# Kernel tuning notes

Measured on AMD Instinct MI355X. Metric: run time of the kernel, lower is better.

## Reference

```python
import jax, jax.numpy as jnp
import numpy as np

WS = 8       # window size
NH = 6       # num heads
SHIFT = 4    # ws//2 since index=1 (shifted)
EPS = 1e-6


def _rel_pos_index(ws):
    coords = np.stack(np.meshgrid(np.arange(ws), np.arange(ws), indexing='ij'))  # (2,ws,ws)
    cf = coords.reshape(2, -1)
    rel = (cf[:, :, None] - cf[:, None, :]).transpose(1, 2, 0)  # (N,N,2)
    rel[..., 0] += ws - 1
    rel[..., 1] += ws - 1
    rel[..., 0] *= 2 * ws - 1
    return rel.sum(-1)  # (N,N) int


def _attn_mask(H, W, ws, shift):
    img = np.zeros((H, W))
    slices = (slice(0, -ws), slice(-ws, -shift), slice(-shift, None))
    cnt = 0
    for h in slices:
        for w in slices:
            img[h, w] = cnt
            cnt += 1
    mw = img.reshape(H // ws, ws, W // ws, ws).transpose(0, 2, 1, 3).reshape(-1, ws * ws)
    am = mw[:, None, :] - mw[:, :, None]  # (nW,N,N): unsqueeze(1) - unsqueeze(2)
    return np.where(am != 0, -100.0, 0.0).astype(np.float32)


def layernorm2d(x, w, b):
    mu = x.mean(1, keepdims=True)
    var = ((x - mu) ** 2).mean(1, keepdims=True)
    y = (x - mu) / jnp.sqrt(var + EPS)
    return w[None, :, None, None] * y + b[None, :, None, None]


def window_partition(x, ws):
    B, C, H, W = x.shape
    x = x.reshape(B, C, H // ws, ws, W // ws, ws)
    return x.transpose(0, 2, 4, 3, 5, 1).reshape(-1, ws * ws, C)


def window_reverse(win, ws, H, W):
    B = win.shape[0] // ((H // ws) * (W // ws))
    x = win.reshape(B, H // ws, W // ws, ws, ws, -1)
    return x.transpose(0, 5, 1, 3, 2, 4).reshape(B, -1, H, W)


def shifted_window_attn(x, qkv_w, qkv_b, proj_w, proj_b, rpb_table):
    B, C, H, W = x.shape
    N = WS * WS
    hd = C // NH
    scale = hd ** -0.5
    # faithful to original: raw reshape BCHW->BHWC (reinterpretation), roll, reshape back
    x = jnp.roll(x.reshape(B, H, W, C), (-SHIFT, -SHIFT), (1, 2)).reshape(B, C, H, W)
    win = window_partition(x, WS)  # (B_, N, C)
    B_ = win.shape[0]
    qkv = (win @ qkv_w + qkv_b).reshape(B_, N, 3, NH, hd).transpose(2, 0, 3, 1, 4)
    q, k, v = qkv[0] * scale, qkv[1], qkv[2]
    attn = jnp.einsum('bhnd,bhmd->bhnm', q, k)  # (B_,NH,N,N)
    rpi = _rel_pos_index(WS)
    bias = rpb_table[rpi.reshape(-1)].reshape(N, N, NH).transpose(2, 0, 1)
    attn = attn + bias[None]
    mask = jnp.asarray(_attn_mask(H, W, WS, SHIFT))  # (nW,N,N)
    nW = mask.shape[0]
    attn = attn.reshape(B_ // nW, nW, NH, N, N) + mask[None, :, None]
    attn = jax.nn.softmax(attn.reshape(B_, NH, N, N), axis=-1)
    out = jnp.einsum('bhnm,bhmd->bhnd', attn, v).transpose(0, 2, 1, 3).reshape(B_, N, C)
    out = out @ proj_w + proj_b
    return window_reverse(out, WS, H, W)


def channel_attention(y, ca_w, ca_b):
    gap = y.mean((2, 3))  # (B,C)
    s = jnp.einsum('bc,oc->bo', gap, ca_w) + ca_b  # 1x1 conv on pooled feature
    return s[:, :, None, None]


def mlp(y, fc1_w, fc1_b, fc2_w, fc2_b):
    B, C, H, W = y.shape
    t = y.transpose(0, 2, 3, 1)  # (B,H,W,C)
    t = jax.nn.gelu(t @ fc1_w + fc1_b, approximate=False)
    t = t @ fc2_w + fc2_b
    return t.transpose(0, 3, 1, 2)


def setup_inputs() -> dict:
    key = jax.random.key(0)
    ks = jax.random.split(key, 8)
    C, H, W, B = 192, 256, 256, 2
    hid = 2 * C
    sc = 0.02
    return {
        'x': jax.random.normal(ks[0], (B, C, H, W), jnp.float32),
        'norm1_w': jnp.ones((C,), jnp.float32),
        'norm1_b': jnp.zeros((C,), jnp.float32),
        'qkv_w': jax.random.normal(ks[1], (C, 3 * C), jnp.float32) * sc,
        'qkv_b': jnp.zeros((3 * C,), jnp.float32),
        'proj_w': jax.random.normal(ks[2], (C, C), jnp.float32) * sc,
        'proj_b': jnp.zeros((C,), jnp.float32),
        'rpb_table': jax.random.normal(ks[3], ((2 * WS - 1) ** 2, NH), jnp.float32) * sc,
        'ca_w': jax.random.normal(ks[4], (C, C), jnp.float32) * sc,
        'ca_b': jnp.zeros((C,), jnp.float32),
        'norm2_w': jnp.ones((C,), jnp.float32),
        'norm2_b': jnp.zeros((C,), jnp.float32),
        'fc1_w': jax.random.normal(ks[5], (C, hid), jnp.float32) * sc,
        'fc1_b': jnp.zeros((hid,), jnp.float32),
        'fc2_w': jax.random.normal(ks[6], (hid, C), jnp.float32) * sc,
        'fc2_b': jnp.zeros((C,), jnp.float32),
    }


def reference(x, norm1_w, norm1_b, qkv_w, qkv_b, proj_w, proj_b, rpb_table,
              ca_w, ca_b, norm2_w, norm2_b, fc1_w, fc1_b, fc2_w, fc2_b):
    y = layernorm2d(x, norm1_w, norm1_b)
    y = shifted_window_attn(y, qkv_w, qkv_b, proj_w, proj_b, rpb_table)
    y = y * channel_attention(y, ca_w, ca_b)
    x = x + y
    y2 = mlp(layernorm2d(x, norm2_w, norm2_b), fc1_w, fc1_b, fc2_w, fc2_b)
    return x + y2
```

## Files before the change

### kernel.cpp

```cpp
#include <hip/hip_runtime.h>
#include <hip/hip_bf16.h>
#include <stdint.h>

#define C_   192
#define H_   256
#define W_   256
#define HW_  65536
#define CHW  12582912
#define NH_  6
#define HID_ 384

typedef __attribute__((ext_vector_type(8))) __bf16 bf16x8;
typedef __attribute__((ext_vector_type(4))) float  fx4;

__device__ __forceinline__ uint16_t f2bf(float f) {
  uint32_t u = __builtin_bit_cast(uint32_t, f);
  u += 0x7fffu + ((u >> 16) & 1u);
  return (uint16_t)(u >> 16);
}
__device__ __forceinline__ float bf2f(uint16_t h) {
  uint32_t u = ((uint32_t)h) << 16;
  return __builtin_bit_cast(float, u);
}
__device__ __forceinline__ uint32_t pk2(float a, float b) {
  return (uint32_t)f2bf(a) | ((uint32_t)f2bf(b) << 16);
}
__device__ __forceinline__ bf16x8 ld8(const uint16_t* p) {
  uint4 v = *reinterpret_cast<const uint4*>(p);
  return __builtin_bit_cast(bf16x8, v);
}
__device__ __forceinline__ fx4 mfma16(bf16x8 a, bf16x8 b, fx4 c) {
  return __builtin_amdgcn_mfma_f32_16x16x32_bf16(a, b, c, 0, 0, 0);
}

__global__ __launch_bounds__(256) void prep_kernel(
    const float* __restrict__ qkv_w, const float* __restrict__ proj_w,
    const float* __restrict__ fc1_w, const float* __restrict__ fc2_w,
    const float* __restrict__ rpb,
    uint16_t* __restrict__ qkv_wt, uint16_t* __restrict__ proj_wt,
    uint16_t* __restrict__ fc1_wt, uint16_t* __restrict__ fc2_wt,
    float* __restrict__ rpbb) {
  int tid = blockIdx.x * 256 + threadIdx.x;
  if (tid < 576 * 192) {
    int f = tid / 192, k = tid % 192;
    qkv_wt[tid] = f2bf(qkv_w[k * 576 + f]);
  }
  int t1 = tid - 576 * 192;
  if (t1 >= 0 && t1 < 192 * 192) {
    int f = t1 / 192, k = t1 % 192;
    proj_wt[t1] = f2bf(proj_w[k * 192 + f]);
  }
  int t2 = t1 - 192 * 192;
  if (t2 >= 0 && t2 < 384 * 192) {
    int f = t2 / 192, k = t2 % 192;
    fc1_wt[t2] = f2bf(fc1_w[k * 384 + f]);
  }
  int t3 = t2 - 384 * 192;
  if (t3 >= 0 && t3 < 192 * 384) {
    int f = t3 / 384, k = t3 % 384;
    fc2_wt[t3] = f2bf(fc2_w[k * 192 + f]);
  }
  int t4 = t3 - 192 * 384;
  if (t4 >= 0 && t4 < 6 * 64 * 64) {
    int h = t4 / 4096, nm = t4 % 4096, n = nm / 64, m = nm % 64;
    int yn = n >> 3, xn = n & 7, ym = m >> 3, xm = m & 7;
    int idx = (yn - ym + 7) * 15 + (xn - xm + 7);
    rpbb[t4] = rpb[idx * NH_ + h];
  }
}

__global__ __launch_bounds__(256) void ln1_stats(const float* __restrict__ x,
                                                 float* __restrict__ mu,
                                                 float* __restrict__ rsig) {
  int t = blockIdx.x * 256 + threadIdx.x;
  int b = t >> 16, hw = t & 65535;
  const float* xp = x + (size_t)b * CHW + hw;
  float s = 0.f, sq = 0.f;
#pragma unroll 8
  for (int c = 0; c < C_; c++) {
    float v = xp[(size_t)c * HW_];
    s += v; sq += v * v;
  }
  float m = s * (1.0f / C_);
  float var = sq * (1.0f / C_) - m * m;
  mu[t] = m;
  rsig[t] = rsqrtf(var + 1e-6f);
}

__global__ __launch_bounds__(256) void ln1_apply_kernel(
    const float* __restrict__ x, const float* __restrict__ mu, const float* __restrict__ rsig,
    const float* __restrict__ n1w, const float* __restrict__ n1b,
    uint16_t* __restrict__ y_tok) {
  __shared__ __attribute__((aligned(16))) uint16_t tile[192 * 66];
  int wg = blockIdx.x;
  int b = wg >> 10, hw0 = (wg & 1023) << 6;
  int t = threadIdx.x;
  const float* xb = x + (size_t)b * CHW;
  const float* mub = mu + b * HW_;
  const float* rsb = rsig + b * HW_;
#pragma unroll 4
  for (int it = 0; it < 48; it++) {
    int id = it * 256 + t;
    int ca = id >> 6, pp = id & 63;
    int g = ca * 65536 + hw0 + pp;
    int h2 = g / 49152;
    int r = g - h2 * 49152;
    int w2 = r / 192;
    int c2 = r - w2 * 192;
    int f = ((h2 + 4) & 255) * 49152 + ((w2 + 4) & 255) * 192 + c2;
    int cnat = f >> 16;
    int hwn = f & 65535;
    float v = (xb[f] - mub[hwn]) * rsb[hwn] * n1w[cnat] + n1b[cnat];
    tile[ca * 66 + pp] = f2bf(v);
  }
  __syncthreads();
  uint16_t* yb = y_tok + ((size_t)(b * HW_ + hw0)) * C_;
#pragma unroll 4
  for (int it = 0; it < 48; it++) {
    int id = it * 256 + t;
    int pp = id / 192, ca = id - pp * 192;
    yb[id] = tile[ca * 66 + pp];
  }
}

__global__ __launch_bounds__(256, 2) void attn_kernel(
    const uint16_t* __restrict__ y_tok, const uint16_t* __restrict__ qkv_wt,
    const float* __restrict__ qkv_b, const uint16_t* __restrict__ proj_wt,
    const float* __restrict__ proj_b, const float* __restrict__ rpbb,
    uint16_t* __restrict__ y_attn) {
  __shared__ __attribute__((aligned(16))) uint16_t Qs[64 * 200];
  __shared__ __attribute__((aligned(16))) uint16_t Ks[64 * 200];
  __shared__ __attribute__((aligned(16))) uint16_t VT[32 * 72];
  __shared__ __attribute__((aligned(16))) uint16_t Ps[64 * 72];
  const int wg = blockIdx.x;
  const int b = wg >> 10, wid = wg & 1023;
  const int wh = wid >> 5, ww = wid & 31;
  const int t = threadIdx.x;
  const int w = t >> 6, l = t & 63;
  const int lane16 = l & 15, quad = l >> 4;
  const int trow = w * 16 + quad * 4;

  bf16x8 afr[4][6];
#pragma unroll
  for (int m = 0; m < 4; m++) {
    const int tok = m * 16 + lane16;
    const uint16_t* ap = y_tok +
        ((size_t)(b * HW_ + (wh * 8 + (tok >> 3)) * W_ + ww * 8 + (tok & 7))) * C_ + quad * 8;
#pragma unroll
    for (int k = 0; k < 6; k++) afr[m][k] = ld8(ap + k * 32);
  }

  const float scale = 0.17677669529663687f;
  uint32_t vpack[3][4][2];

#pragma unroll
  for (int j = 0; j < 3; j++) {
    const int nt = w + 4 * j;
    const uint16_t* bp = qkv_wt + (nt * 16 + lane16) * C_ + quad * 8;
    bf16x8 bfr[6];
#pragma unroll
    for (int k = 0; k < 6; k++) bfr[k] = ld8(bp + k * 32);
    fx4 acc[4];
#pragma unroll
    for (int m = 0; m < 4; m++) acc[m] = fx4{0.f, 0.f, 0.f, 0.f};
#pragma unroll
    for (int k = 0; k < 6; k++)
#pragma unroll
      for (int m = 0; m < 4; m++) acc[m] = mfma16(afr[m][k], bfr[k], acc[m]);
    const int f = nt * 16 + lane16;
    const float bias = qkv_b[f];
#pragma unroll
    for (int m = 0; m < 4; m++)
#pragma unroll
      for (int r = 0; r < 4; r++)
        Qs[(m * 16 + quad * 4 + r) * 200 + f] = f2bf((acc[m][r] + bias) * scale);
  }
#pragma unroll
  for (int j = 3; j < 6; j++) {
    const int nt = w + 4 * j;
    const uint16_t* bp = qkv_wt + (nt * 16 + lane16) * C_ + quad * 8;
    bf16x8 bfr[6];
#pragma unroll
    for (int k = 0; k < 6; k++) bfr[k] = ld8(bp + k * 32);
    fx4 acc[4];
#pragma unroll
    for (int m = 0; m < 4; m++) acc[m] = fx4{0.f, 0.f, 0.f, 0.f};
#pragma unroll
    for (int k = 0; k < 6; k++)
#pragma unroll
      for (int m = 0; m < 4; m++) acc[m] = mfma16(afr[m][k], bfr[k], acc[m]);
    const int f = nt * 16 + lane16;
    const float bias = qkv_b[f];
#pragma unroll
    for (int m = 0; m < 4; m++)
#pragma unroll
      for (int r = 0; r < 4; r++)
        Ks[(m * 16 + quad * 4 + r) * 200 + (f - 192)] = f2bf(acc[m][r] + bias);
  }
#pragma unroll
  for (int j = 6; j < 9; j++) {
    const int nt = w + 4 * j;
    const uint16_t* bp = qkv_wt + (nt * 16 + lane16) * C_ + quad * 8;
    bf16x8 bfr[6];
#pragma unroll
    for (int k = 0; k < 6; k++) bfr[k] = ld8(bp + k * 32);
    fx4 acc[4];
#pragma unroll
    for (int m = 0; m < 4; m++) acc[m] = fx4{0.f, 0.f, 0.f, 0.f};
#pragma unroll
    for (int k = 0; k < 6; k++)
#pragma unroll
      for (int m = 0; m < 4; m++) acc[m] = mfma16(afr[m][k], bfr[k], acc[m]);
    const float bias = qkv_b[nt * 16 + lane16];
    const int jv = j - 6;
#pragma unroll
    for (int m = 0; m < 4; m++) {
      vpack[jv][m][0] = pk2(acc[m][0] + bias, acc[m][1] + bias);
      vpack[jv][m][1] = pk2(acc[m][2] + bias, acc[m][3] + bias);
    }
  }

  const bool whe = (wh == 31), wwe = (ww == 31);

  for (int h = 0; h < 6; h++) {
    __syncthreads();
    {
      const int vt0 = 2 * h, vt1 = 2 * h + 1;
      if (w == (vt0 & 3)) {
        const int jv = vt0 >> 2;
#pragma unroll
        for (int m = 0; m < 4; m++) {
          uint2 vv; vv.x = vpack[jv][m][0]; vv.y = vpack[jv][m][1];
          *reinterpret_cast<uint2*>(&VT[lane16 * 72 + m * 16 + quad * 4]) = vv;
        }
      }
      if (w == (vt1 & 3)) {
        const int jv = vt1 >> 2;
#pragma unroll
        for (int m = 0; m < 4; m++) {
          uint2 vv; vv.x = vpack[jv][m][0]; vv.y = vpack[jv][m][1];
          *reinterpret_cast<uint2*>(&VT[(16 + lane16) * 72 + m * 16 + quad * 4]) = vv;
        }
      }
    }
    __syncthreads();

    const bf16x8 qa = ld8(&Qs[(w * 16 + lane16) * 200 + h * 32 + quad * 8]);
    fx4 sacc[4];
#pragma unroll
    for (int nt = 0; nt < 4; nt++) {
      const bf16x8 kb = ld8(&Ks[(nt * 16 + lane16) * 200 + h * 32 + quad * 8]);
      fx4 z = {0.f, 0.f, 0.f, 0.f};
      sacc[nt] = mfma16(qa, kb, z);
    }
    const float* rb = rpbb + h * 4096;
#pragma unroll
    for (int nt = 0; nt < 4; nt++) {
      const int ct = nt * 16 + lane16;
      const bool rbc = whe && ((ct >> 3) >= 4);
      const bool cbc = wwe && ((ct & 7) >= 4);
#pragma unroll
      for (int r = 0; r < 4; r++) {
        const int rt = trow + r;
        const bool rbr = whe && ((rt >> 3) >= 4);
        const bool cbr = wwe && ((rt & 7) >= 4);
        float v = sacc[nt][r] + rb[rt * 64 + ct];
        if (rbr != rbc || cbr != cbc) v -= 100.f;
        sacc[nt][r] = v;
      }
    }
    float sm[4];
#pragma unroll
    for (int r = 0; r < 4; r++) {
      float m = fmaxf(fmaxf(sacc[0][r], sacc[1][r]), fmaxf(sacc[2][r], sacc[3][r]));
      m = fmaxf(m, __shfl_xor(m, 1));
      m = fmaxf(m, __shfl_xor(m, 2));
      m = fmaxf(m, __shfl_xor(m, 4));
      m = fmaxf(m, __shfl_xor(m, 8));
      float s0 = 0.f;
#pragma unroll
      for (int nt = 0; nt < 4; nt++) {
        float e = exp2f((sacc[nt][r] - m) * 1.4426950408889634f);
        sacc[nt][r] = e; s0 += e;
      }
      s0 += __shfl_xor(s0, 1);
      s0 += __shfl_xor(s0, 2);
      s0 += __shfl_xor(s0, 4);
      s0 += __shfl_xor(s0, 8);
      sm[r] = s0;
    }
#pragma unroll
    for (int nt = 0; nt < 4; nt++)
#pragma unroll
      for (int r = 0; r < 4; r++)
        Ps[(trow + r) * 72 + nt * 16 + lane16] = f2bf(sacc[nt][r]);
    fx4 o0 = {0.f, 0.f, 0.f, 0.f}, o1 = {0.f, 0.f, 0.f, 0.f};
#pragma unroll
    for (int ks2 = 0; ks2 < 2; ks2++) {
      const bf16x8 pa = ld8(&Ps[(w * 16 + lane16) * 72 + ks2 * 32 + quad * 8]);
      const bf16x8 v0 = ld8(&VT[(lane16) * 72 + ks2 * 32 + quad * 8]);
      const bf16x8 v1 = ld8(&VT[(16 + lane16) * 72 + ks2 * 32 + quad * 8]);
      o0 = mfma16(pa, v0, o0);
      o1 = mfma16(pa, v1, o1);
    }
#pragma unroll
    for (int r = 0; r < 4; r++) {
      const float inv = 1.0f / sm[r];
      Qs[(trow + r) * 200 + h * 32 + lane16] = f2bf(o0[r] * inv);
      Qs[(trow + r) * 200 + h * 32 + 16 + lane16] = f2bf(o1[r] * inv);
    }
  }
  __syncthreads();

  bf16x8 ofr[4][6];
#pragma unroll
  for (int m = 0; m < 4; m++)
#pragma unroll
    for (int k = 0; k < 6; k++)
      ofr[m][k] = ld8(&Qs[(m * 16 + lane16) * 200 + k * 32 + quad * 8]);

  uint16_t* yb = y_attn + (size_t)b * HW_ * C_;
  uint32_t obase[4][4];
#pragma unroll
  for (int m = 0; m < 4; m++)
#pragma unroll
    for (int r = 0; r < 4; r++) {
      const int tok = m * 16 + quad * 4 + r;
      obase[m][r] = (uint32_t)(((wh * 8 + (tok >> 3)) * W_ + ww * 8 + (tok & 7)) * C_);
    }
#pragma unroll
  for (int j = 0; j < 3; j++) {
    const int nt = w + 4 * j;
    const uint16_t* bp = proj_wt + (nt * 16 + lane16) * C_ + quad * 8;
    bf16x8 bfr[6];
#pragma unroll
    for (int k = 0; k < 6; k++) bfr[k] = ld8(bp + k * 32);
    fx4 acc[4];
#pragma unroll
    for (int m = 0; m < 4; m++) acc[m] = fx4{0.f, 0.f, 0.f, 0.f};
#pragma unroll
    for (int k = 0; k < 6; k++)
#pragma unroll
      for (int m = 0; m < 4; m++) acc[m] = mfma16(ofr[m][k], bfr[k], acc[m]);
    const float pb = proj_b[nt * 16 + lane16];
#pragma unroll
    for (int m = 0; m < 4; m++)
#pragma unroll
      for (int r = 0; r < 4; r++)
        yb[obase[m][r] + nt * 16 + lane16] = f2bf(acc[m][r] + pb);
  }
}

__global__ __launch_bounds__(256) void gap_partial(const uint16_t* __restrict__ y_attn,
                                                   float* __restrict__ part) {
  int wg = blockIdx.x;
  int b = wg >> 9, sl = wg & 511;
  int t = threadIdx.x;
  if (t < 192) {
    size_t base = ((size_t)(b * HW_ + sl * 128)) * C_ + t;
    float s = 0.f;
#pragma unroll 8
    for (int r = 0; r < 128; r++) s += bf2f(y_attn[base + (size_t)r * C_]);
    part[wg * 192 + t] = s;
  }
}

__global__ __launch_bounds__(768) void ca_s_kernel(const float* __restrict__ part,
                                                   const float* __restrict__ ca_w,
                                                   const float* __restrict__ ca_b,
                                                   float* __restrict__ sbuf) {
  int b = blockIdx.x;
  int t = threadIdx.x;
  __shared__ float red[768];
  __shared__ float gap[192];
  int g = t / 192, c = t - g * 192;
  float s = 0.f;
#pragma unroll 8
  for (int i = g; i < 512; i += 4) s += part[(b * 512 + i) * 192 + c];
  red[t] = s;
  __syncthreads();
  if (t < 192)
    gap[t] = (red[t] + red[t + 192] + red[t + 384] + red[t + 576]) * (1.0f / 65536.0f);
  __syncthreads();
  if (t < 192) {
    float acc = ca_b[t];
#pragma unroll 8
    for (int c2 = 0; c2 < 192; c2++) acc += gap[c2] * ca_w[t * 192 + c2];
    sbuf[b * 192 + t] = acc;
  }
}

__global__ __launch_bounds__(256, 3) void resid_ln2(
    const float* __restrict__ x, const uint16_t* __restrict__ y_attn,
    const float* __restrict__ sbuf, const float* __restrict__ n2w,
    const float* __restrict__ n2b, float* __restrict__ x_new,
    uint16_t* __restrict__ t2) {
  __shared__ __attribute__((aligned(16))) float tile[192 * 66];
  __shared__ float red[512];
  __shared__ float mus[128];
  int wg = blockIdx.x;
  int b = wg >> 10, hw0 = (wg & 1023) << 6;
  int t = threadIdx.x;
#pragma unroll 4
  for (int it = 0; it < 48; it++) {
    int id = it * 256 + t;
    int c = id >> 6, p = id & 63;
    tile[c * 66 + p] = x[(size_t)b * CHW + (size_t)c * HW_ + hw0 + p];
  }
  __syncthreads();
#pragma unroll 4
  for (int it = 0; it < 48; it++) {
    int id = it * 256 + t;
    int p = id / 192, c = id - p * 192;
    float y = bf2f(y_attn[((size_t)(b * HW_ + hw0 + p)) * C_ + c]);
    tile[c * 66 + p] += sbuf[b * 192 + c] * y;
  }
  __syncthreads();
  {
    int p = t & 63, g = t >> 6;
    float s = 0.f, sq = 0.f;
    for (int c = g * 48; c < g * 48 + 48; c++) {
      float v = tile[c * 66 + p];
      s += v; sq += v * v;
    }
    red[g * 64 + p] = s;
    red[256 + g * 64 + p] = sq;
  }
  __syncthreads();
  if (t < 64) {
    float ss = red[t] + red[64 + t] + red[128 + t] + red[192 + t];
    float qq = red[256 + t] + red[320 + t] + red[384 + t] + red[448 + t];
    float m = ss * (1.0f / C_);
    float var = qq * (1.0f / C_) - m * m;
    mus[t] = m;
    mus[64 + t] = rsqrtf(var + 1e-6f);
  }
  __syncthreads();
#pragma unroll 4
  for (int it = 0; it < 48; it++) {
    int id = it * 256 + t;
    int c = id >> 6, p = id & 63;
    x_new[(size_t)b * CHW + (size_t)c * HW_ + hw0 + p] = tile[c * 66 + p];
  }
#pragma unroll 4
  for (int it = 0; it < 48; it++) {
    int id = it * 256 + t;
    int p = id / 192, c = id - p * 192;
    float v = (tile[c * 66 + p] - mus[p]) * mus[64 + p] * n2w[c] + n2b[c];
    t2[((size_t)(b * HW_ + hw0 + p)) * C_ + c] = f2bf(v);
  }
}

__global__ __launch_bounds__(256, 2) void mlp_kernel(
    const uint16_t* __restrict__ t2, const uint16_t* __restrict__ fc1_wt,
    const float* __restrict__ fc1_b, const uint16_t* __restrict__ fc2_wt,
    const float* __restrict__ fc2_b, const float* __restrict__ x_new,
    float* __restrict__ out) {
  __shared__ __attribute__((aligned(16))) char smem[64 * 392 * 2];
  uint16_t* hbuf = (uint16_t*)smem;
  uint16_t* obuf = (uint16_t*)smem;
  int wg = blockIdx.x;
  int b = wg >> 10, hw0 = (wg & 1023) << 6;
  int t = threadIdx.x;
  int w = t >> 6, l = t & 63;
  int lane16 = l & 15, quad = l >> 4;

  bf16x8 afr[4][6];
  const uint16_t* ab = t2 + ((size_t)(b * HW_ + hw0)) * C_;
#pragma unroll
  for (int m = 0; m < 4; m++) {
    const uint16_t* ap = ab + (m * 16 + lane16) * C_ + quad * 8;
#pragma unroll
    for (int k = 0; k < 6; k++) afr[m][k] = ld8(ap + k * 32);
  }

#pragma unroll
  for (int j = 0; j < 6; j++) {
    const int nt = w + 4 * j;
    const uint16_t* bp = fc1_wt + (nt * 16 + lane16) * C_ + quad * 8;
    bf16x8 bfr[6];
#pragma unroll
    for (int k = 0; k < 6; k++) bfr[k] = ld8(bp + k * 32);
    fx4 acc[4];
#pragma unroll
    for (int m = 0; m < 4; m++) acc[m] = fx4{0.f, 0.f, 0.f, 0.f};
#pragma unroll
    for (int k = 0; k < 6; k++)
#pragma unroll
      for (int m = 0; m < 4; m++) acc[m] = mfma16(afr[m][k], bfr[k], acc[m]);
    const float bias = fc1_b[nt * 16 + lane16];
#pragma unroll
    for (int m = 0; m < 4; m++)
#pragma unroll
      for (int r = 0; r < 4; r++) {
        float v = acc[m][r] + bias;
        float ge = 0.5f * v * (1.0f + erff(v * 0.7071067811865476f));
        hbuf[(m * 16 + quad * 4 + r) * 392 + nt * 16 + lane16] = f2bf(ge);
      }
  }
  __syncthreads();

  fx4 acc2[3][4];
#pragma unroll
  for (int j = 0; j < 3; j++)
#pragma unroll
    for (int m = 0; m < 4; m++) acc2[j][m] = fx4{0.f, 0.f, 0.f, 0.f};
#pragma unroll
  for (int kc = 0; kc < 4; kc++) {
    bf16x8 ha[4][3];
#pragma unroll
    for (int m = 0; m < 4; m++)
#pragma unroll
      for (int kk = 0; kk < 3; kk++)
        ha[m][kk] = ld8(&hbuf[(m * 16 + lane16) * 392 + kc * 96 + kk * 32 + quad * 8]);
#pragma unroll
    for (int j = 0; j < 3; j++) {
      const int nt = w + 4 * j;
      const uint16_t* bp = fc2_wt + (nt * 16 + lane16) * HID_ + kc * 96 + quad * 8;
#pragma unroll
      for (int kk = 0; kk < 3; kk++) {
        const bf16x8 bb = ld8(bp + kk * 32);
#pragma unroll
        for (int m = 0; m < 4; m++) acc2[j][m] = mfma16(ha[m][kk], bb, acc2[j][m]);
      }
    }
  }
  __syncthreads();

#pragma unroll
  for (int j = 0; j < 3; j++) {
    const int nt = w + 4 * j;
    const float bias = fc2_b[nt * 16 + lane16];
#pragma unroll
    for (int m = 0; m < 4; m++) {
      uint2 vv;
      vv.x = pk2(acc2[j][m][0] + bias, acc2[j][m][1] + bias);
      vv.y = pk2(acc2[j][m][2] + bias, acc2[j][m][3] + bias);
      *reinterpret_cast<uint2*>(&obuf[(nt * 16 + lane16) * 68 + m * 16 + quad * 4]) = vv;
    }
  }
  __syncthreads();
#pragma unroll 4
  for (int it = 0; it < 48; it++) {
    int id = it * 256 + t;
    int c = id >> 6, p = id & 63;
    size_t gi = (size_t)b * CHW + (size_t)c * HW_ + hw0 + p;
    out[gi] = x_new[gi] + bf2f(obuf[c * 68 + p]);
  }
}

extern "C" void kernel_launch(void* const* d_in, const int* in_sizes, int n_in,
                              void* d_out, int out_size, void* d_ws, size_t ws_size,
                              hipStream_t stream) {
  const float* x      = (const float*)d_in[0];
  const float* n1w    = (const float*)d_in[1];
  const float* n1b    = (const float*)d_in[2];
  const float* qkv_w  = (const float*)d_in[3];
  const float* qkv_b  = (const float*)d_in[4];
  const float* proj_w = (const float*)d_in[5];
  const float* proj_b = (const float*)d_in[6];
  const float* rpb    = (const float*)d_in[7];
  const float* ca_w   = (const float*)d_in[8];
  const float* ca_b   = (const float*)d_in[9];
  const float* n2w    = (const float*)d_in[10];
  const float* n2b    = (const float*)d_in[11];
  const float* fc1_w  = (const float*)d_in[12];
  const float* fc1_b  = (const float*)d_in[13];
  const float* fc2_w  = (const float*)d_in[14];
  const float* fc2_b  = (const float*)d_in[15];
  float* out = (float*)d_out;

  char* ws = (char*)d_ws;
  uint16_t* y_tok   = (uint16_t*)(ws + 0);
  uint16_t* y_attn  = (uint16_t*)(ws + 50331648);
  float*    x_new   = (float*)   (ws + 100663296);
  uint16_t* t2      = y_tok;
  float*    part    = x_new;
  float*    mu      = (float*)   (ws + 201326592);
  float*    rsig    = (float*)   (ws + 201850880);
  uint16_t* qkv_wt  = (uint16_t*)(ws + 202375168);
  uint16_t* proj_wt = (uint16_t*)(ws + 202596352);
  uint16_t* fc1_wt  = (uint16_t*)(ws + 202670080);
  uint16_t* fc2_wt  = (uint16_t*)(ws + 202817536);
  float*    rpbb    = (float*)   (ws + 202964992);
  float*    sbuf    = (float*)   (ws + 203063296);

  hipLaunchKernelGGL(prep_kernel, dim3(1248), dim3(256), 0, stream,
                     qkv_w, proj_w, fc1_w, fc2_w, rpb, qkv_wt, proj_wt, fc1_wt, fc2_wt, rpbb);
  hipLaunchKernelGGL(ln1_stats, dim3(512), dim3(256), 0, stream, x, mu, rsig);
  hipLaunchKernelGGL(ln1_apply_kernel, dim3(2048), dim3(256), 0, stream,
                     x, mu, rsig, n1w, n1b, y_tok);
  hipLaunchKernelGGL(attn_kernel, dim3(2048), dim3(256), 0, stream,
                     y_tok, qkv_wt, qkv_b, proj_wt, proj_b, rpbb, y_attn);
  hipLaunchKernelGGL(gap_partial, dim3(1024), dim3(256), 0, stream, y_attn, part);
  hipLaunchKernelGGL(ca_s_kernel, dim3(2), dim3(768), 0, stream, part, ca_w, ca_b, sbuf);
  hipLaunchKernelGGL(resid_ln2, dim3(2048), dim3(256), 0, stream,
                     x, y_attn, sbuf, n2w, n2b, x_new, t2);
  hipLaunchKernelGGL(mlp_kernel, dim3(2048), dim3(256), 0, stream,
                     t2, fc1_wt, fc1_b, fc2_wt, fc2_b, x_new, out);
}
```

Before: 575.2 us.

## Fuse GAP partial sums into attention epilogue and recompute residual in MLP

The global-average-pool partial sums are now produced in the attention kernel's projection epilogue using wave shuffles, which removes the separate gap_partial pass that re-read y_attn. resid_ln2 no longer writes x_new to memory. Instead, the MLP kernel recomputes the residual by re-reading x and y_attn and scaling by the channel-attention vector. This trades a 48MB fp32 write and a later 48MB read for a 24MB bf16 re-read. The fc2 output is also kept in fp32 in LDS, which makes the shared-memory tile larger, while launch bounds are raised to 3.

```diff
diff --git a/kernel.cpp b/kernel.cpp
--- a/kernel.cpp
+++ b/kernel.cpp
@@ -127,7 +127,7 @@
     const uint16_t* __restrict__ y_tok, const uint16_t* __restrict__ qkv_wt,
     const float* __restrict__ qkv_b, const uint16_t* __restrict__ proj_wt,
     const float* __restrict__ proj_b, const float* __restrict__ rpbb,
-    uint16_t* __restrict__ y_attn) {
+    uint16_t* __restrict__ y_attn, float* __restrict__ part) {
   __shared__ __attribute__((aligned(16))) uint16_t Qs[64 * 200];
   __shared__ __attribute__((aligned(16))) uint16_t Ks[64 * 200];
   __shared__ __attribute__((aligned(16))) uint16_t VT[32 * 72];
@@ -343,25 +343,18 @@
 #pragma unroll
       for (int m = 0; m < 4; m++) acc[m] = mfma16(ofr[m][k], bfr[k], acc[m]);
     const float pb = proj_b[nt * 16 + lane16];
+    float cs = 0.f;
 #pragma unroll
     for (int m = 0; m < 4; m++)
 #pragma unroll
-      for (int r = 0; r < 4; r++)
-        yb[obase[m][r] + nt * 16 + lane16] = f2bf(acc[m][r] + pb);
-  }
-}
-
-__global__ __launch_bounds__(256) void gap_partial(const uint16_t* __restrict__ y_attn,
-                                                   float* __restrict__ part) {
-  int wg = blockIdx.x;
-  int b = wg >> 9, sl = wg & 511;
-  int t = threadIdx.x;
-  if (t < 192) {
-    size_t base = ((size_t)(b * HW_ + sl * 128)) * C_ + t;
-    float s = 0.f;
-#pragma unroll 8
-    for (int r = 0; r < 128; r++) s += bf2f(y_attn[base + (size_t)r * C_]);
-    part[wg * 192 + t] = s;
+      for (int r = 0; r < 4; r++) {
+        const float v = acc[m][r] + pb;
+        yb[obase[m][r] + nt * 16 + lane16] = f2bf(v);
+        cs += v;
+      }
+    cs += __shfl_xor(cs, 16);
+    cs += __shfl_xor(cs, 32);
+    if (l < 16) part[(size_t)wg * 192 + nt * 16 + lane16] = cs;
   }
 }
 
@@ -376,7 +369,7 @@
   int g = t / 192, c = t - g * 192;
   float s = 0.f;
 #pragma unroll 8
-  for (int i = g; i < 512; i += 4) s += part[(b * 512 + i) * 192 + c];
+  for (int i = g; i < 1024; i += 4) s += part[((size_t)b * 1024 + i) * 192 + c];
   red[t] = s;
   __syncthreads();
   if (t < 192)
@@ -393,8 +386,7 @@
 __global__ __launch_bounds__(256, 3) void resid_ln2(
     const float* __restrict__ x, const uint16_t* __restrict__ y_attn,
     const float* __restrict__ sbuf, const float* __restrict__ n2w,
-    const float* __restrict__ n2b, float* __restrict__ x_new,
-    uint16_t* __restrict__ t2) {
+    const float* __restrict__ n2b, uint16_t* __restrict__ t2) {
   __shared__ __attribute__((aligned(16))) float tile[192 * 66];
   __shared__ float red[512];
   __shared__ float mus[128];
@@ -439,31 +431,28 @@
 #pragma unroll 4
   for (int it = 0; it < 48; it++) {
     int id = it * 256 + t;
-    int c = id >> 6, p = id & 63;
-    x_new[(size_t)b * CHW + (size_t)c * HW_ + hw0 + p] = tile[c * 66 + p];
-  }
-#pragma unroll 4
-  for (int it = 0; it < 48; it++) {
-    int id = it * 256 + t;
     int p = id / 192, c = id - p * 192;
     float v = (tile[c * 66 + p] - mus[p]) * mus[64 + p] * n2w[c] + n2b[c];
     t2[((size_t)(b * HW_ + hw0 + p)) * C_ + c] = f2bf(v);
   }
 }
 
-__global__ __launch_bounds__(256, 2) void mlp_kernel(
+__global__ __launch_bounds__(256, 3) void mlp_kernel(
     const uint16_t* __restrict__ t2, const uint16_t* __restrict__ fc1_wt,
     const float* __restrict__ fc1_b, const uint16_t* __restrict__ fc2_wt,
-    const float* __restrict__ fc2_b, const float* __restrict__ x_new,
+    const float* __restrict__ fc2_b, const float* __restrict__ x,
+    const uint16_t* __restrict__ y_attn, const float* __restrict__ sbuf,
     float* __restrict__ out) {
-  __shared__ __attribute__((aligned(16))) char smem[64 * 392 * 2];
+  __shared__ __attribute__((aligned(16))) char smem[192 * 66 * 4];
+  __shared__ float sarr[192];
   uint16_t* hbuf = (uint16_t*)smem;
-  uint16_t* obuf = (uint16_t*)smem;
+  float* ftile = (float*)smem;
   int wg = blockIdx.x;
   int b = wg >> 10, hw0 = (wg & 1023) << 6;
   int t = threadIdx.x;
   int w = t >> 6, l = t & 63;
   int lane16 = l & 15, quad = l >> 4;
+  if (t < 192) sarr[t] = sbuf[b * 192 + t];
 
   bf16x8 afr[4][6];
   const uint16_t* ab = t2 + ((size_t)(b * HW_ + hw0)) * C_;
@@ -533,11 +522,20 @@
     const float bias = fc2_b[nt * 16 + lane16];
 #pragma unroll
     for (int m = 0; m < 4; m++) {
-      uint2 vv;
-      vv.x = pk2(acc2[j][m][0] + bias, acc2[j][m][1] + bias);
-      vv.y = pk2(acc2[j][m][2] + bias, acc2[j][m][3] + bias);
-      *reinterpret_cast<uint2*>(&obuf[(nt * 16 + lane16) * 68 + m * 16 + quad * 4]) = vv;
-    }
+      float* fp = &ftile[(nt * 16 + lane16) * 66 + m * 16 + quad * 4];
+      float2 a = {acc2[j][m][0] + bias, acc2[j][m][1] + bias};
+      float2 b2 = {acc2[j][m][2] + bias, acc2[j][m][3] + bias};
+      *reinterpret_cast<float2*>(fp) = a;
+      *reinterpret_cast<float2*>(fp + 2) = b2;
+    }
+  }
+  __syncthreads();
+#pragma unroll 4
+  for (int it = 0; it < 48; it++) {
+    int id = it * 256 + t;
+    int p = id / 192, c = id - p * 192;
+    float y = bf2f(y_attn[((size_t)(b * HW_ + hw0 + p)) * C_ + c]);
+    ftile[c * 66 + p] += sarr[c] * y;
   }
   __syncthreads();
 #pragma unroll 4
@@ -545,7 +543,7 @@
     int id = it * 256 + t;
     int c = id >> 6, p = id & 63;
     size_t gi = (size_t)b * CHW + (size_t)c * HW_ + hw0 + p;
-    out[gi] = x_new[gi] + bf2f(obuf[c * 68 + p]);
+    out[gi] = x[gi] + ftile[c * 66 + p];
   }
 }
 
@@ -573,17 +571,16 @@
   char* ws = (char*)d_ws;
   uint16_t* y_tok   = (uint16_t*)(ws + 0);
   uint16_t* y_attn  = (uint16_t*)(ws + 50331648);
-  float*    x_new   = (float*)   (ws + 100663296);
   uint16_t* t2      = y_tok;
-  float*    part    = x_new;
-  float*    mu      = (float*)   (ws + 201326592);
-  float*    rsig    = (float*)   (ws + 201850880);
-  uint16_t* qkv_wt  = (uint16_t*)(ws + 202375168);
-  uint16_t* proj_wt = (uint16_t*)(ws + 202596352);
-  uint16_t* fc1_wt  = (uint16_t*)(ws + 202670080);
-  uint16_t* fc2_wt  = (uint16_t*)(ws + 202817536);
-  float*    rpbb    = (float*)   (ws + 202964992);
-  float*    sbuf    = (float*)   (ws + 203063296);
+  float*    mu      = (float*)   (ws + 100663296);
+  float*    rsig    = (float*)   (ws + 101187584);
+  uint16_t* qkv_wt  = (uint16_t*)(ws + 101711872);
+  uint16_t* proj_wt = (uint16_t*)(ws + 101933056);
+  uint16_t* fc1_wt  = (uint16_t*)(ws + 102006784);
+  uint16_t* fc2_wt  = (uint16_t*)(ws + 102154240);
+  float*    rpbb    = (float*)   (ws + 102301696);
+  float*    part    = (float*)   (ws + 102400000);
+  float*    sbuf    = (float*)   (ws + 103972864);
 
   hipLaunchKernelGGL(prep_kernel, dim3(1248), dim3(256), 0, stream,
                      qkv_w, proj_w, fc1_w, fc2_w, rpb, qkv_wt, proj_wt, fc1_wt, fc2_wt, rpbb);
@@ -591,11 +588,10 @@
   hipLaunchKernelGGL(ln1_apply_kernel, dim3(2048), dim3(256), 0, stream,
                      x, mu, rsig, n1w, n1b, y_tok);
   hipLaunchKernelGGL(attn_kernel, dim3(2048), dim3(256), 0, stream,
-                     y_tok, qkv_wt, qkv_b, proj_wt, proj_b, rpbb, y_attn);
-  hipLaunchKernelGGL(gap_partial, dim3(1024), dim3(256), 0, stream, y_attn, part);
+                     y_tok, qkv_wt, qkv_b, proj_wt, proj_b, rpbb, y_attn, part);
   hipLaunchKernelGGL(ca_s_kernel, dim3(2), dim3(768), 0, stream, part, ca_w, ca_b, sbuf);
   hipLaunchKernelGGL(resid_ln2, dim3(2048), dim3(256), 0, stream,
-                     x, y_attn, sbuf, n2w, n2b, x_new, t2);
+                     x, y_attn, sbuf, n2w, n2b, t2);
   hipLaunchKernelGGL(mlp_kernel, dim3(2048), dim3(256), 0, stream,
-                     t2, fc1_wt, fc1_b, fc2_wt, fc2_b, x_new, out);
-}
+                     t2, fc1_wt, fc1_b, fc2_wt, fc2_b, x, y_attn, sbuf, out);
+}
```

After: 556.9 us. 3.2% less time.
